# Kernel optimization log

Hardware: AMD Instinct MI355X
Metric: run time of the kernel (lower is better)

Reference implementation:

```python
import jax, jax.numpy as jnp
import numpy as np

E, D, H, K, DIL, T = 8, 768, 3072, 3, 1, 16384


def _conv1d(x, w, b, dilation):
    # x: [1, C_in, L]; w: [C_out, C_in, K]; torch Conv1d with SAME padding
    pad = dilation * (w.shape[-1] - 1) // 2
    y = jax.lax.conv_general_dilated(
        x, w, window_strides=(1,), padding=[(pad, pad)],
        rhs_dilation=(dilation,), dimension_numbers=("NCH", "OIH", "NCH"))
    return y + b[None, :, None]


def setup_inputs() -> dict:
    key = jax.random.key(0)
    k0, k1, k2, k3, k4 = jax.random.split(key, 5)
    inp = jax.random.normal(k0, (T, D), dtype=jnp.float32)
    fwd_expert_count = jnp.full((E,), T // E, dtype=jnp.int32)
    w1 = jax.random.normal(k1, (E, H, D, K), dtype=jnp.float32) * (1.0 / np.sqrt(D * K))
    b1 = jax.random.normal(k2, (E, H), dtype=jnp.float32) * 0.01
    w2 = jax.random.normal(k3, (E, D, H, K), dtype=jnp.float32) * (1.0 / np.sqrt(H * K))
    b2 = jax.random.normal(k4, (E, D), dtype=jnp.float32) * 0.01
    return {"inp": inp, "fwd_expert_count": fwd_expert_count,
            "w1": w1, "b1": b1, "w2": w2, "b2": b2}


def reference(inp, fwd_expert_count, w1, b1, w2, b2):
    # counts define static per-expert segment lengths (constants w.r.t. compute graph)
    counts = np.asarray(jax.device_get(fwd_expert_count))
    x = inp.T[None]  # [1, D, T]
    outs, idx = [], 0
    for i in range(counts.shape[0]):
        n = int(counts[i])
        if n > 0:
            outs.append(_conv1d(x[:, :, idx:idx + n], w1[i], b1[i], DIL))
            idx += n
    h = jax.nn.gelu(jnp.concatenate(outs, axis=2), approximate=False)  # [1, H, T]
    outs, idx = [], 0
    for i in range(counts.shape[0]):
        n = int(counts[i])
        if n > 0:
            outs.append(_conv1d(h[:, :, idx:idx + n], w2[i], b2[i], DIL))
            idx += n
    y = jnp.concatenate(outs, axis=2)[0]  # [D, T]
    return y.T  # [T, D]
```

## Files before the change

### kernel.cpp

```cpp
#include <hip/hip_runtime.h>
#include <hip/hip_bf16.h>
#include <cstdint>

#define E_   8
#define D_   768
#define H_   3072
#define T_   16384
#define SEG  2048
#define PSEG (SEG + 2)

typedef __attribute__((ext_vector_type(8))) __bf16 bf16x8;
typedef __attribute__((ext_vector_type(4))) float f32x4;
typedef __attribute__((ext_vector_type(4))) unsigned int u32x4;

__device__ inline unsigned short f2bf(float f) {
  union { float f; unsigned int u; } v; v.f = f;
  unsigned int u = v.u;
  u += 0x7fffu + ((u >> 16) & 1u);
  return (unsigned short)(u >> 16);
}

__device__ inline float gelu_fast(float x) {
  const float a = -2.302118131f;
  const float b = -0.102944213f;
  float z = x * __builtin_fmaf(b, x * x, a);
  float e = __builtin_amdgcn_exp2f(z);
  return x * __builtin_amdgcn_rcpf(1.0f + e);
}

__device__ inline unsigned cvt_pk_bf16(float lo, float hi) {
  unsigned r;
  asm("v_cvt_pk_bf16_f32 %0, %1, %2" : "=v"(r) : "v"(lo), "v"(hi));
  return r;
}

__device__ inline void gload16(const unsigned short* g, unsigned short* l) {
  __builtin_amdgcn_global_load_lds(
      (const __attribute__((address_space(1))) unsigned int*)g,
      (__attribute__((address_space(3))) unsigned int*)l, 16, 0, 0);
}

template <int C>
__device__ inline void cvt_w_body(const float* __restrict__ in,
                                  unsigned short* __restrict__ out, int i) {
  constexpr int C8 = C / 8;
  const int row = i / C8;
  const int cq = i - row * C8;
  const float* src = in + ((size_t)row * C + cq * 8) * 3;
  unsigned short* dst = out + (size_t)row * 3 * C + cq * 8;
  f32x4 v[6];
#pragma unroll
  for (int j = 0; j < 6; ++j) v[j] = *(const f32x4*)(src + j * 4);
  const float* f = (const float*)v;
#pragma unroll
  for (int k = 0; k < 3; ++k) {
    u32x4 w;
#pragma unroll
    for (int j = 0; j < 4; ++j)
      w[j] = (unsigned)f2bf(f[(2 * j) * 3 + k]) |
             ((unsigned)f2bf(f[(2 * j + 1) * 3 + k]) << 16);
    *(u32x4*)(dst + k * C) = w;
  }
}

__global__ __launch_bounds__(256) void prep_kernel(
    const float* __restrict__ inp, const float* __restrict__ w1,
    const float* __restrict__ w2, unsigned short* __restrict__ Xp,
    unsigned short* __restrict__ Hp, unsigned short* __restrict__ W1T,
    unsigned short* __restrict__ W2T) {
  const int b = blockIdx.x;
  const int tid = threadIdx.x;
  if (b < 32) {
    unsigned short* buf = (b < 16) ? Xp : Hp;
    const int C = (b < 16) ? D_ : H_;
    const int bb = b & 15;
    const size_t row = (size_t)(bb >> 1) * PSEG + (bb & 1) * (PSEG - 1);
    for (int c = tid; c < C; c += 256) buf[row * C + c] = 0;
  } else if (b < 32 + 6144) {
    const int i = (b - 32) * 256 + tid;
    const int elem = i * 8;
    const int row = elem / D_;
    const int col = elem - row * D_;
    const int prow = (row >> 11) * PSEG + 1 + (row & (SEG - 1));
    const float* p = inp + (size_t)row * D_ + col;
    u32x4 v;
#pragma unroll
    for (int j = 0; j < 4; ++j)
      v[j] = (unsigned)f2bf(p[2 * j]) | ((unsigned)f2bf(p[2 * j + 1]) << 16);
    *(u32x4*)(Xp + (size_t)prow * D_ + col) = v;
  } else if (b < 32 + 6144 + 9216) {
    cvt_w_body<D_>(w1, W1T, (b - 6176) * 256 + tid);
  } else {
    cvt_w_body<H_>(w2, W2T, (b - 15392) * 256 + tid);
  }
}

template <int CIN, int COUT, bool DO_GELU>
__global__ __launch_bounds__(512, 2) void conv_gemm8_kernel(
    const unsigned short* __restrict__ A,
    const unsigned short* __restrict__ Bt,
    const float* __restrict__ bias,
    void* __restrict__ Out) {
  __shared__ __align__(16) unsigned short lds[65536];

  constexpr int CSTEPS = CIN / 64;
  constexpr int NT = 3 * CSTEPS;
  constexpr int NTN = COUT / 256;

  const int tid  = threadIdx.x;
  const int wid  = tid >> 6, lane = tid & 63;
  const int wm   = wid >> 2, wn = wid & 3;

  const int bid = blockIdx.x;
  const int e   = bid & 7;
  const int rem = bid >> 3;
  const int mc  = rem / (4 * NTN);
  const int r2  = rem - mc * 4 * NTN;
  const int m0  = (mc * 4 + (r2 & 3)) * 256;
  const int n0  = (r2 >> 2) * 256;

  const int rowoff = tid >> 3;
  const int psrc   = ((lane & 7) ^ (lane >> 3)) * 8;
  const int ko     = (lane >> 4) * 16;
  const int ax     = (lane & 7) << 4;
  const int l15    = lane & 15;

  const int koax0 = ko ^ ax;
  const int koax1 = (64 | ko) ^ ax;
  const char* pA0 = (const char*)lds + wm * 16384 + l15 * 128 + koax0;
  const char* pA1 = (const char*)lds + wm * 16384 + l15 * 128 + koax1;
  const char* pB0 = (const char*)lds + 65536 + (wn >> 1) * 16384 +
                    ((wn & 1) * 64 + l15) * 128 + koax0;
  const char* pB1 = (const char*)lds + 65536 + (wn >> 1) * 16384 +
                    ((wn & 1) * 64 + l15) * 128 + koax1;

  const unsigned short* aU = A + ((size_t)e * PSEG + m0) * CIN;
  const unsigned short* bU = Bt + (size_t)(e * COUT + n0) * 3 * CIN;
  const int avo = rowoff * CIN + psrc;
  const int bvo = rowoff * 3 * CIN + psrc;
  size_t aOff = 0, bOff = 0;

  f32x4 acc[8][4];
#pragma unroll
  for (int n = 0; n < 4; ++n) {
    const float bv = bias[e * COUT + n0 + wn * 64 + n * 16 + l15];
#pragma unroll
    for (int m = 0; m < 8; ++m) acc[m][n] = (f32x4){bv, bv, bv, bv};
  }

#define STAGE_A(BUF_, part_) do {                                                    \
    _Pragma("unroll")                                                                \
    for (int ii_ = 0; ii_ < 2; ++ii_)                                                \
      gload16(aU + aOff + avo + (ii_ * 128 + (part_) * 64) * CIN,                    \
              (unsigned short*)((char*)lds + (BUF_) * 32768 + ii_ * 16384 +          \
                                (part_) * 8192 + wid * 1024 + lane * 16));           \
  } while (0)

#define STAGE_B(BUF_, h_) do {                                                       \
    _Pragma("unroll")                                                                \
    for (int ii_ = 0; ii_ < 2; ++ii_)                                                \
      gload16(bU + bOff + bvo + ((h_) * 128 + ii_ * 64) * 3 * CIN,                   \
              (unsigned short*)((char*)lds + 65536 + (BUF_) * 32768 + (h_) * 16384 + \
                                ii_ * 8192 + wid * 1024 + lane * 16));               \
  } while (0)

#define ADVA(nx_) do { if ((nx_) < NT) aOff += 64; } while (0)
#define ADVB(nx_) do { if ((nx_) < NT) bOff += 64; } while (0)

#define FULLBAR() do { asm volatile("" ::: "memory");                                \
                       __builtin_amdgcn_s_barrier();                                 \
                       asm volatile("" ::: "memory"); } while (0)
#define VM6() asm volatile("s_waitcnt vmcnt(6)" ::: "memory")
#define VM4() asm volatile("s_waitcnt vmcnt(4)" ::: "memory")
#define VM_NONE()

#define RA(buf_, mq_, s_, raA_, raB_, RB_) do {                                      \
    const char* pAx_ = (s_) ? pA1 : pA0;                                             \
    if (RB_) {                                                                       \
      const char* pBx_ = (s_) ? pB1 : pB0;                                           \
      _Pragma("unroll")                                                              \
      for (int n_ = 0; n_ < 4; ++n_)                                                 \
        raB_[n_] = *(const bf16x8*)(pBx_ + (buf_) * 32768 + n_ * 2048);              \
    }                                                                                \
    _Pragma("unroll")                                                                \
    for (int mi_ = 0; mi_ < 4; ++mi_)                                                \
      raA_[mi_] = *(const bf16x8*)(pAx_ + (buf_) * 32768 + ((mq_) * 4 + mi_) * 2048);\
  } while (0)

#define PHASE(raBuf_, raMq_, raS_, raA_, raB_, RB_, useA_, useB_, mq_, STAGE_STMT, VMW_) \
  do {                                                                               \
    FULLBAR();                                                                       \
    RA(raBuf_, raMq_, raS_, raA_, raB_, RB_);                                        \
    STAGE_STMT;                                                                      \
    __builtin_amdgcn_s_setprio(1);                                                   \
    _Pragma("unroll")                                                                \
    for (int mi_ = 0; mi_ < 4; ++mi_)                                                \
      _Pragma("unroll")                                                              \
      for (int n_ = 0; n_ < 4; ++n_)                                                 \
        acc[(mq_) * 4 + mi_][n_] = __builtin_amdgcn_mfma_f32_16x16x32_bf16(          \
            useA_[mi_], useB_[n_], acc[(mq_) * 4 + mi_][n_], 0, 0, 0);               \
    __builtin_amdgcn_s_setprio(0);                                                   \
    VMW_();                                                                          \
  } while (0)

  STAGE_B(0, 0); STAGE_B(0, 1); ADVB(1);
  STAGE_A(0, 0); STAGE_A(0, 1); ADVA(1);
  STAGE_B(1, 0); STAGE_B(1, 1); ADVB(2);
  VM6();
  FULLBAR();

  bf16x8 aFA[4], aFB[4], bFA[4], bFB[4];
  RA(0, 0, 0, aFA, bFA, 1);

  int kt0 = 0;
#pragma unroll 1
  for (int it = 0; it < NT / 2; ++it, kt0 += 2) {
    PHASE(0, 0, 1, aFB, bFB, 1, aFA, bFA, 0, STAGE_A(1, 0), VM6);
    PHASE(0, 1, 0, aFA, bFA, 0, aFB, bFB, 0, { STAGE_A(1, 1); ADVA(kt0 + 2); }, VM_NONE);
    PHASE(0, 1, 1, aFB, bFB, 0, aFA, bFA, 1, STAGE_B(0, 0), VM4);
    PHASE(1, 0, 0, aFA, bFA, 1, aFB, bFB, 1, { STAGE_B(0, 1); ADVB(kt0 + 3); }, VM_NONE);
    PHASE(1, 0, 1, aFB, bFB, 1, aFA, bFA, 0, STAGE_A(0, 0), VM6);
    PHASE(1, 1, 0, aFA, bFA, 0, aFB, bFB, 0, { STAGE_A(0, 1); ADVA(kt0 + 3); }, VM_NONE);
    PHASE(1, 1, 1, aFB, bFB, 0, aFA, bFA, 1, STAGE_B(1, 0), VM4);
    PHASE(0, 0, 0, aFA, bFA, 1, aFB, bFB, 1, { STAGE_B(1, 1); ADVB(kt0 + 4); }, VM_NONE);
  }

  asm volatile("s_waitcnt vmcnt(0)" ::: "memory");

#undef PHASE
#undef RA
#undef STAGE_A
#undef STAGE_B
#undef ADVA
#undef ADVB

#pragma unroll
  for (int m = 0; m < 8; ++m) {
    const int rowb = m0 + wm * 128 + m * 16 + ((lane >> 4) << 2);
#pragma unroll
    for (int n = 0; n < 4; ++n) {
      const int col = n0 + wn * 64 + n * 16 + l15;
      if (DO_GELU) {
        unsigned short* ob = (unsigned short*)Out +
                             ((size_t)e * PSEG + 1 + rowb) * COUT + col;
#pragma unroll
        for (int i = 0; i < 4; i += 2) {
          const unsigned pk = cvt_pk_bf16(gelu_fast(acc[m][n][i]),
                                          gelu_fast(acc[m][n][i + 1]));
          ob[(size_t)i * COUT] = (unsigned short)pk;
          ob[(size_t)(i + 1) * COUT] = (unsigned short)(pk >> 16);
        }
      } else {
        float* ob = (float*)Out + ((size_t)e * SEG + rowb) * COUT + col;
#pragma unroll
        for (int i = 0; i < 4; ++i) ob[(size_t)i * COUT] = acc[m][n][i];
      }
    }
  }
#undef FULLBAR
#undef VM6
#undef VM4
#undef VM_NONE
}

template <int CIN, int COUT>
__global__ __launch_bounds__(512, 2) void conv_gemm_n192_kernel(
    const unsigned short* __restrict__ A,
    const unsigned short* __restrict__ Bt,
    const float* __restrict__ bias,
    float* __restrict__ Out) {
  __shared__ __align__(16) unsigned short lds[57344];

  constexpr int CSTEPS = CIN / 64;
  constexpr int NT = 3 * CSTEPS;

  const int tid  = threadIdx.x;
  const int wid  = tid >> 6, lane = tid & 63;
  const int wm   = wid >> 2, wn = wid & 3;

  const int bid = blockIdx.x;
  const int e   = bid & 7;
  const int rem = bid >> 3;
  const int m0  = (rem & 7) * 256;
  const int n0  = (rem >> 3) * 192;

  const int rowoff = tid >> 3;
  const int psrc   = ((lane & 7) ^ (lane >> 3)) * 8;
  const int ko     = (lane >> 4) * 16;
  const int ax     = (lane & 7) << 4;
  const int l15    = lane & 15;

  const int koax0 = ko ^ ax;
  const int koax1 = (64 | ko) ^ ax;
  const char* pA0 = (const char*)lds + wm * 16384 + l15 * 128 + koax0;
  const char* pA1 = (const char*)lds + wm * 16384 + l15 * 128 + koax1;
  const char* pB0 = (const char*)lds + 65536 + wn * 6144 + l15 * 128 + koax0;
  const char* pB1 = (const char*)lds + 65536 + wn * 6144 + l15 * 128 + koax1;

  const unsigned short* aU = A + ((size_t)e * PSEG + m0) * CIN;
  const unsigned short* bU = Bt + (size_t)(e * COUT + n0) * 3 * CIN;
  const int avo = rowoff * CIN + psrc;
  const int bvo = rowoff * 3 * CIN + psrc;
  size_t aOff = 0, bOff = 0;

  f32x4 acc[8][3];
#pragma unroll
  for (int n = 0; n < 3; ++n) {
    const float bv = bias[e * COUT + n0 + wn * 48 + n * 16 + l15];
#pragma unroll
    for (int m = 0; m < 8; ++m) acc[m][n] = (f32x4){bv, bv, bv, bv};
  }

#define ADVA(nx_) do { if ((nx_) < NT) aOff += 64; } while (0)
#define ADVB(nx_) do { if ((nx_) < NT) bOff += 64; } while (0)

#define STAGE_A2(BUF_, slot_)                                                        \
  gload16(aU + aOff + avo + ((slot_) * 64) * CIN,                                    \
          (unsigned short*)((char*)lds + (BUF_) * 32768 + (slot_) * 8192 +           \
                            wid * 1024 + lane * 16))
#define STAGE_B2(BUF_, slot_)                                                        \
  gload16(bU + bOff + bvo + ((slot_) * 64) * 3 * CIN,                                \
          (unsigned short*)((char*)lds + 65536 + (BUF_) * 24576 + (slot_) * 8192 +   \
                            wid * 1024 + lane * 16))

#define FULLBAR() do { asm volatile("" ::: "memory");                                \
                       __builtin_amdgcn_s_barrier();                                 \
                       asm volatile("" ::: "memory"); } while (0)
#define VM3() asm volatile("s_waitcnt vmcnt(3)" ::: "memory")
#define VM2() asm volatile("s_waitcnt vmcnt(2)" ::: "memory")

#define RA_A2(buf_, mq_, s_, dst_) do {                                              \
    const char* pAx_ = (s_) ? pA1 : pA0;                                             \
    _Pragma("unroll")                                                                \
    for (int mi_ = 0; mi_ < 4; ++mi_)                                                \
      dst_[mi_] = *(const bf16x8*)(pAx_ + (buf_) * 32768 + ((mq_) * 4 + mi_) * 2048);\
  } while (0)

#define RA_B2(buf_, s_, dst_) do {                                                   \
    const char* pBx_ = (s_) ? pB1 : pB0;                                             \
    _Pragma("unroll")                                                                \
    for (int n_ = 0; n_ < 3; ++n_)                                                   \
      dst_[n_] = *(const bf16x8*)(pBx_ + (buf_) * 24576 + n_ * 2048);                \
  } while (0)

#define MFMA12(mq_, aU_, bU_) do {                                                   \
    __builtin_amdgcn_s_setprio(1);                                                   \
    _Pragma("unroll")                                                                \
    for (int mi_ = 0; mi_ < 4; ++mi_)                                                \
      _Pragma("unroll")                                                              \
      for (int n_ = 0; n_ < 3; ++n_)                                                 \
        acc[(mq_) * 4 + mi_][n_] = __builtin_amdgcn_mfma_f32_16x16x32_bf16(          \
            aU_[mi_], bU_[n_], acc[(mq_) * 4 + mi_][n_], 0, 0, 0);                   \
    __builtin_amdgcn_s_setprio(0);                                                   \
  } while (0)

  STAGE_A2(0, 0); STAGE_A2(0, 1); STAGE_A2(0, 2); STAGE_A2(0, 3); ADVA(1);
  STAGE_B2(0, 0); STAGE_B2(0, 1); STAGE_B2(0, 2); ADVB(1);
  STAGE_B2(1, 0); STAGE_B2(1, 1); STAGE_B2(1, 2); ADVB(2);
  VM3();
  FULLBAR();

  bf16x8 aX[4], aY[4], bF0[3], bF1[3];
  RA_A2(0, 0, 0, aX);
  RA_B2(0, 0, bF0);

  int kt0 = 0;
#pragma unroll 1
  for (int it = 0; it < NT / 2; ++it, kt0 += 2) {
    FULLBAR(); RA_A2(0, 0, 1, aY); RA_B2(0, 1, bF1);
               STAGE_A2(1, 0); STAGE_A2(1, 1); STAGE_A2(1, 2); STAGE_A2(1, 3);
               ADVA(kt0 + 2); MFMA12(0, aX, bF0);
    FULLBAR(); RA_A2(0, 1, 0, aX); MFMA12(0, aY, bF1);
    FULLBAR(); RA_A2(0, 1, 1, aY); STAGE_B2(0, 0); STAGE_B2(0, 1);
               MFMA12(1, aX, bF0); VM2();
    FULLBAR(); RA_A2(1, 0, 0, aX); RA_B2(1, 0, bF0); STAGE_B2(0, 2);
               ADVB(kt0 + 3); MFMA12(1, aY, bF1);
    FULLBAR(); RA_A2(1, 0, 1, aY); RA_B2(1, 1, bF1);
               STAGE_A2(0, 0); STAGE_A2(0, 1); STAGE_A2(0, 2); STAGE_A2(0, 3);
               ADVA(kt0 + 3); MFMA12(0, aX, bF0);
    FULLBAR(); RA_A2(1, 1, 0, aX); MFMA12(0, aY, bF1);
    FULLBAR(); RA_A2(1, 1, 1, aY); STAGE_B2(1, 0); STAGE_B2(1, 1);
               MFMA12(1, aX, bF0); VM2();
    FULLBAR(); RA_A2(0, 0, 0, aX); RA_B2(0, 0, bF0); STAGE_B2(1, 2);
               ADVB(kt0 + 4); MFMA12(1, aY, bF1);
  }

  asm volatile("s_waitcnt vmcnt(0)" ::: "memory");

#undef MFMA12
#undef RA_A2
#undef RA_B2
#undef STAGE_A2
#undef STAGE_B2
#undef ADVA
#undef ADVB
#undef FULLBAR
#undef VM3
#undef VM2

#pragma unroll
  for (int m = 0; m < 8; ++m) {
    const int rowb = m0 + wm * 128 + m * 16 + ((lane >> 4) << 2);
#pragma unroll
    for (int n = 0; n < 3; ++n) {
      const int col = n0 + wn * 48 + n * 16 + l15;
      float* ob = Out + ((size_t)e * SEG + rowb) * COUT + col;
#pragma unroll
      for (int i = 0; i < 4; ++i) ob[(size_t)i * COUT] = acc[m][n][i];
    }
  }
}

extern "C" void kernel_launch(void* const* d_in, const int* in_sizes, int n_in,
                              void* d_out, int out_size, void* d_ws, size_t ws_size,
                              hipStream_t stream) {
  const float* inp = (const float*)d_in[0];
  const float* w1 = (const float*)d_in[2];
  const float* b1 = (const float*)d_in[3];
  const float* w2 = (const float*)d_in[4];
  const float* b2 = (const float*)d_in[5];
  float* out = (float*)d_out;
  char* ws = (char*)d_ws;

  const size_t szXp = (size_t)E_ * PSEG * D_ * 2;
  const size_t szHp = (size_t)E_ * PSEG * H_ * 2;
  const size_t szW1 = (size_t)E_ * H_ * 3 * D_ * 2;
  const size_t szW2 = (size_t)E_ * D_ * 3 * H_ * 2;

  unsigned short* Xp  = (unsigned short*)ws;
  unsigned short* Hp  = (unsigned short*)(ws + szXp);
  unsigned short* W1T = (unsigned short*)(ws + szXp + szHp);
  unsigned short* W2T = (unsigned short*)(ws + szXp + szHp + szW1);

  if (ws_size < szXp + szHp + szW1 + szW2) return;

  constexpr int PREP_BLOCKS = 32 + (T_ * D_ / 8 / 256)
                            + (E_ * H_) * (D_ / 8) / 256
                            + (E_ * D_) * (H_ / 8) / 256;
  prep_kernel<<<PREP_BLOCKS, 256, 0, stream>>>(inp, w1, w2, Xp, Hp, W1T, W2T);

  constexpr int NWG1 = (H_ / 256) * (SEG / 256) * E_;
  constexpr int NWG2 = (D_ / 192) * (SEG / 256) * E_;
  conv_gemm8_kernel<D_, H_, true>
      <<<NWG1, 512, 0, stream>>>(Xp, W1T, b1, Hp);
  conv_gemm_n192_kernel<H_, D_>
      <<<NWG2, 512, 0, stream>>>(Hp, W2T, b2, out);
}
```

Before: 508.3 us.

## Restructure GEMM main loop into barrier-separated load and MFMA phases

Replaces the ping-pong A-fragment register scheme (aX/aY), where LDS reads for the next step overlapped the current MFMA block, with a single fragment set. Each step now reads LDS, issues global staging, then runs its MFMAs between two full barriers. The vmcnt waits move to after the MFMA blocks. This cuts register pressure and simplifies the schedule, possibly in a ping-pong style across waves. The cost is about twice as many barriers and less overlap of LDS reads with MFMA inside a wave.

```diff
diff --git a/kernel.cpp b/kernel.cpp
--- a/kernel.cpp
+++ b/kernel.cpp
@@ -327,7 +327,6 @@
                        __builtin_amdgcn_s_barrier();                                 \
                        asm volatile("" ::: "memory"); } while (0)
 #define VM3() asm volatile("s_waitcnt vmcnt(3)" ::: "memory")
-#define VM2() asm volatile("s_waitcnt vmcnt(2)" ::: "memory")
 
 #define RA_A2(buf_, mq_, s_, dst_) do {                                              \
     const char* pAx_ = (s_) ? pA1 : pA0;                                             \
@@ -360,29 +359,40 @@
   VM3();
   FULLBAR();
 
-  bf16x8 aX[4], aY[4], bF0[3], bF1[3];
-  RA_A2(0, 0, 0, aX);
-  RA_B2(0, 0, bF0);
+  bf16x8 aF[4], bF0[3], bF1[3];
 
   int kt0 = 0;
 #pragma unroll 1
   for (int it = 0; it < NT / 2; ++it, kt0 += 2) {
-    FULLBAR(); RA_A2(0, 0, 1, aY); RA_B2(0, 1, bF1);
-               STAGE_A2(1, 0); STAGE_A2(1, 1); STAGE_A2(1, 2); STAGE_A2(1, 3);
-               ADVA(kt0 + 2); MFMA12(0, aX, bF0);
-    FULLBAR(); RA_A2(0, 1, 0, aX); MFMA12(0, aY, bF1);
-    FULLBAR(); RA_A2(0, 1, 1, aY); STAGE_B2(0, 0); STAGE_B2(0, 1);
-               MFMA12(1, aX, bF0); VM2();
-    FULLBAR(); RA_A2(1, 0, 0, aX); RA_B2(1, 0, bF0); STAGE_B2(0, 2);
-               ADVB(kt0 + 3); MFMA12(1, aY, bF1);
-    FULLBAR(); RA_A2(1, 0, 1, aY); RA_B2(1, 1, bF1);
-               STAGE_A2(0, 0); STAGE_A2(0, 1); STAGE_A2(0, 2); STAGE_A2(0, 3);
-               ADVA(kt0 + 3); MFMA12(0, aX, bF0);
-    FULLBAR(); RA_A2(1, 1, 0, aX); MFMA12(0, aY, bF1);
-    FULLBAR(); RA_A2(1, 1, 1, aY); STAGE_B2(1, 0); STAGE_B2(1, 1);
-               MFMA12(1, aX, bF0); VM2();
-    FULLBAR(); RA_A2(0, 0, 0, aX); RA_B2(0, 0, bF0); STAGE_B2(1, 2);
-               ADVB(kt0 + 4); MFMA12(1, aY, bF1);
+    RA_A2(0, 0, 0, aF); RA_B2(0, 0, bF0);
+    STAGE_A2(1, 0); STAGE_A2(1, 1); STAGE_A2(1, 2); STAGE_A2(1, 3); ADVA(kt0 + 2);
+    FULLBAR(); MFMA12(0, aF, bF0); FULLBAR();
+
+    RA_A2(0, 0, 1, aF); RA_B2(0, 1, bF1);
+    FULLBAR(); MFMA12(0, aF, bF1); FULLBAR();
+
+    RA_A2(0, 1, 0, aF);
+    STAGE_B2(0, 0); STAGE_B2(0, 1);
+    FULLBAR(); MFMA12(1, aF, bF0); FULLBAR();
+
+    RA_A2(0, 1, 1, aF);
+    STAGE_B2(0, 2); ADVB(kt0 + 3);
+    FULLBAR(); MFMA12(1, aF, bF1); VM3(); FULLBAR();
+
+    RA_A2(1, 0, 0, aF); RA_B2(1, 0, bF0);
+    STAGE_A2(0, 0); STAGE_A2(0, 1); STAGE_A2(0, 2); STAGE_A2(0, 3); ADVA(kt0 + 3);
+    FULLBAR(); MFMA12(0, aF, bF0); FULLBAR();
+
+    RA_A2(1, 0, 1, aF); RA_B2(1, 1, bF1);
+    FULLBAR(); MFMA12(0, aF, bF1); FULLBAR();
+
+    RA_A2(1, 1, 0, aF);
+    STAGE_B2(1, 0); STAGE_B2(1, 1);
+    FULLBAR(); MFMA12(1, aF, bF0); FULLBAR();
+
+    RA_A2(1, 1, 1, aF);
+    STAGE_B2(1, 2); ADVB(kt0 + 4);
+    FULLBAR(); MFMA12(1, aF, bF1); VM3(); FULLBAR();
   }
 
   asm volatile("s_waitcnt vmcnt(0)" ::: "memory");
@@ -396,7 +406,6 @@
 #undef ADVB
 #undef FULLBAR
 #undef VM3
-#undef VM2
 
 #pragma unroll
   for (int m = 0; m < 8; ++m) {
```

After: 521.8 us. +2.6%, slower.
